# Performance work log

Measured on AMD Instinct MI355X. Metric: run time of the kernel, lower is better.

Reference implementation:

```python
import jax, jax.numpy as jnp
import numpy as np

B, S, D = 2, 2048, 2048
H, HD = 16, 128


def _rope_cos_sin(seq_len, head_dim, base=10000.0):
    inv_freq = 1.0 / (base ** (np.arange(0, head_dim, 2, dtype=np.float32) / head_dim))
    t = np.arange(seq_len, dtype=np.float32)
    freqs = np.outer(t, inv_freq)                      # [S, HD/2]
    emb = np.concatenate([freqs, freqs], axis=-1)      # [S, HD]
    return jnp.asarray(np.cos(emb)), jnp.asarray(np.sin(emb))


def setup_inputs() -> dict:
    key = jax.random.key(0)
    k1, k2, k3 = jax.random.split(key, 3)
    hidden_states = jax.random.normal(k1, (B, S, D), dtype=jnp.float32)
    cos, sin = _rope_cos_sin(S, HD)
    # qkv weight: [3, H*HD, D] as in CastedLinear(batch_output_dims=(3,))
    w_qkv = jax.random.normal(k2, (3, H * HD, D), dtype=jnp.float32) * (1.0 / D ** 0.5)
    w_o = jax.random.normal(k3, (D, H * HD), dtype=jnp.float32) * (1.0 / (H * HD) ** 0.5)
    return {"hidden_states": hidden_states, "cos": cos, "sin": sin, "w_qkv": w_qkv, "w_o": w_o}


def _rotate_half(x):
    x1, x2 = jnp.split(x, 2, axis=-1)
    return jnp.concatenate([-x2, x1], axis=-1)


def _apply_rope(x, cos, sin):
    # x: [B, S, H, HD]; cos/sin: [S, HD] -> broadcast over heads via [:, None, :]
    return x * cos[:, None, :] + _rotate_half(x) * sin[:, None, :]


def reference(hidden_states, cos, sin, w_qkv, w_o):
    # fused QKV projection: weight flattened to [3*H*HD, D]
    qkv = jnp.einsum('bsd,fd->bsf', hidden_states, w_qkv.reshape(-1, D))  # [B,S,3*H*HD]
    # rearrange '... (h hd) -> ... h hd' with h=H  ->  [B,S,H,3*HD], then chunk
    qkv = qkv.reshape(B, S, H, 3 * HD)
    q, k, v = jnp.split(qkv, 3, axis=-1)          # each [B,S,H,HD]
    q = _apply_rope(q, cos, sin)
    k = _apply_rope(k, cos, sin)
    # SDPA, causal
    scale = 1.0 / jnp.sqrt(jnp.asarray(HD, dtype=q.dtype))
    scores = jnp.einsum('bshd,bthd->bhst', q, k) * scale      # [B,H,S,S]
    causal = jnp.tril(jnp.ones((S, S), dtype=bool))
    scores = jnp.where(causal, scores, jnp.asarray(-jnp.inf, dtype=scores.dtype))
    probs = jax.nn.softmax(scores, axis=-1)
    attn = jnp.einsum('bhst,bthd->bshd', probs, v)            # [B,S,H,HD]
    attn = attn.reshape(B, S, H * HD)
    return jnp.einsum('bsf,df->bsd', attn, w_o)               # [B,S,D]
```

## Files before the change

kernel.cpp:

```cpp
#include <hip/hip_runtime.h>

typedef unsigned short u16;
typedef unsigned int u32;
typedef __bf16 bf16x8 __attribute__((ext_vector_type(8)));
typedef float f32x4 __attribute__((ext_vector_type(4)));


__device__ __forceinline__ u16 f2bf(float x) {
  __bf16 h = (__bf16)x;
  return __builtin_bit_cast(u16, h);
}

__device__ __forceinline__ void async_copy16(void* lds, const void* g) {
  __builtin_amdgcn_global_load_lds((const __attribute__((address_space(1))) void*)g,
                                   (__attribute__((address_space(3))) void*)lds, 16, 0, 0);
}

__global__ __launch_bounds__(256) void cast_all(const float* __restrict__ hidden,
                                                const float* __restrict__ wqkv,
                                                const float* __restrict__ wo,
                                                u16* __restrict__ xb,
                                                u16* __restrict__ wqb,
                                                u16* __restrict__ wob) {
  int i = blockIdx.x * 256 + threadIdx.x;
  const float* s;
  u16* d;
  int off;
  if (i < 2097152) { s = hidden; d = xb; off = i; }
  else if (i < 2097152 + 3145728) { s = wqkv; d = wqb; off = i - 2097152; }
  else { s = wo; d = wob; off = i - (2097152 + 3145728); }
  float4 v = ((const float4*)s)[off];
  ushort4 o;
  o.x = f2bf(v.x); o.y = f2bf(v.y); o.z = f2bf(v.z); o.w = f2bf(v.w);
  ((ushort4*)d)[off] = o;
}


__device__ __forceinline__ void lda_ks(bf16x8 (&af)[4][2], const u16* base, int row, int c,
                                       int ks) {
#pragma unroll
  for (int mf = 0; mf < 4; mf++) af[mf][ks] = *(const bf16x8*)(base + (row + mf * 16) * 64 + c);
}

__device__ __forceinline__ void ldb_ks(bf16x8 (&bfr)[2][2], const u16* base, int row, int c,
                                       int ks) {
#pragma unroll
  for (int nf = 0; nf < 2; nf++) bfr[nf][ks] = *(const bf16x8*)(base + (row + nf * 16) * 64 + c);
}

#define FENCE() asm volatile("" ::: "memory")
#define LGKM0() asm volatile("s_waitcnt lgkmcnt(0)" ::: "memory")
#define LGKM2() asm volatile("s_waitcnt lgkmcnt(2)" ::: "memory")
#define LGKM4() asm volatile("s_waitcnt lgkmcnt(4)" ::: "memory")
#define LGKM6() asm volatile("s_waitcnt lgkmcnt(6)" ::: "memory")
#define VMW6() asm volatile("s_waitcnt vmcnt(6)" ::: "memory")
#define VMW0() asm volatile("s_waitcnt vmcnt(0)" ::: "memory")
#define BAR() __builtin_amdgcn_s_barrier()
#define SBAR() __builtin_amdgcn_sched_barrier(0)

#define MFMA_H(MH, NH, KS)                                                               \
  _Pragma("unroll") for (int mf = 0; mf < 4; mf++)                                       \
  _Pragma("unroll") for (int nf = 0; nf < 2; nf++)                                       \
      acc[(MH)*4 + mf][(NH)*2 + nf] = __builtin_amdgcn_mfma_f32_16x16x32_bf16(           \
          af[mf][KS], bfr[nf][KS], acc[(MH)*4 + mf][(NH)*2 + nf], 0, 0, 0);

#define PH_SPLIT(MH, NH, W1, TAIL)      \
  BAR();                                \
  W1; SBAR();                           \
  __builtin_amdgcn_s_setprio(1);        \
  MFMA_H(MH, NH, 0);                    \
  LGKM0(); SBAR();                      \
  MFMA_H(MH, NH, 1);                    \
  __builtin_amdgcn_s_setprio(0);        \
  TAIL;                                 \
  FENCE(); BAR()

#define STG_A(DB, H, KT)                                                                   \
  {                                                                                        \
    async_copy16(ldsA + (DB)*32768 + ((H)*64 + w8) * 128, Ag + aoff[H][0] + (KT)*128);     \
    async_copy16(ldsA + (DB)*32768 + (128 + (H)*64 + w8) * 128, Ag + aoff[H][1] + (KT)*128); \
  }
#define STG_B(DB, H, KT)                                                                   \
  {                                                                                        \
    async_copy16(ldsB + (DB)*32768 + ((H)*64 + w8) * 128, Bg + boff[H][0] + (KT)*128);     \
    async_copy16(ldsB + (DB)*32768 + (128 + (H)*64 + w8) * 128, Bg + boff[H][1] + (KT)*128); \
  }

template <bool MORE>
__device__ __forceinline__ void qkv_iter(const u16* As, const u16* Bs, char* ldsA, char* ldsB,
                                         const char* Ag, const char* Bg,
                                         const u32 (&aoff)[2][2], const u32 (&boff)[2][2],
                                         int w8, int arow0, int brow0, int c0, int c1,
                                         int k1, int k2, int k3,
                                         bf16x8 (&af)[4][2], bf16x8 (&bfr)[2][2],
                                         f32x4 (&acc)[8][4]) {
  const int arow1 = arow0 + 256;
  const int brow1 = brow0 + 256;
  lda_ks(af, As, arow0, c0, 0); ldb_ks(bfr, Bs, brow0, c0, 0); FENCE();
  lda_ks(af, As, arow0, c1, 1); ldb_ks(bfr, Bs, brow0, c1, 1); FENCE();
  STG_B(1, 0, k1);
  PH_SPLIT(0, 0, LGKM6(), (void)0);
  ldb_ks(bfr, Bs, brow0 + 64, c0, 0); FENCE();
  ldb_ks(bfr, Bs, brow0 + 64, c1, 1); FENCE();
  if (MORE) { STG_A(0, 0, k2); }
  PH_SPLIT(0, 1, LGKM2(), (void)0);
  lda_ks(af, As, arow0 + 64, c0, 0); FENCE();
  lda_ks(af, As, arow0 + 64, c1, 1); FENCE();
  if (MORE) { STG_B(0, 1, k2); }
  PH_SPLIT(1, 1, LGKM4(), (void)0);
  ldb_ks(bfr, Bs, brow0, c0, 0); FENCE();
  ldb_ks(bfr, Bs, brow0, c1, 1); FENCE();
  if (MORE) { STG_A(0, 1, k2); }
  if (MORE) { PH_SPLIT(1, 0, LGKM2(), VMW6()); } else { PH_SPLIT(1, 0, LGKM2(), VMW0()); }
  lda_ks(af, As, arow1, c0, 0); ldb_ks(bfr, Bs, brow1, c0, 0); FENCE();
  lda_ks(af, As, arow1, c1, 1); ldb_ks(bfr, Bs, brow1, c1, 1); FENCE();
  if (MORE) { STG_B(0, 0, k2); }
  PH_SPLIT(0, 0, LGKM6(), (void)0);
  ldb_ks(bfr, Bs, brow1 + 64, c0, 0); FENCE();
  ldb_ks(bfr, Bs, brow1 + 64, c1, 1); FENCE();
  if (MORE) { STG_A(1, 0, k3); }
  PH_SPLIT(0, 1, LGKM2(), (void)0);
  lda_ks(af, As, arow1 + 64, c0, 0); FENCE();
  lda_ks(af, As, arow1 + 64, c1, 1); FENCE();
  if (MORE) { STG_B(1, 1, k3); }
  PH_SPLIT(1, 1, LGKM4(), (void)0);
  ldb_ks(bfr, Bs, brow1, c0, 0); FENCE();
  ldb_ks(bfr, Bs, brow1, c1, 1); FENCE();
  if (MORE) { STG_A(1, 1, k3); }
  if (MORE) { PH_SPLIT(1, 0, LGKM2(), VMW6()); } else { PH_SPLIT(1, 0, LGKM2(), (void)0); }
}

__global__ __launch_bounds__(512, 2) void gemm_qkv(const u16* __restrict__ A,
                                                   const u16* __restrict__ W,
                                                   const float* __restrict__ cosb,
                                                   const float* __restrict__ sinb,
                                                   u16* __restrict__ Qb,
                                                   u16* __restrict__ Kb,
                                                   u16* __restrict__ Vt) {
  extern __shared__ u16 smem[];
  u16* As = smem;
  u16* Bs = smem + 32768;
  char* ldsA = (char*)As;
  char* ldsB = (char*)Bs;
  const char* Ag = (const char*)A;
  const char* Bg = (const char*)W;

  const int tid = threadIdx.x;
  const int lane = tid & 63;
  const int w = tid >> 6;
  const int wm = w >> 2;
  const int wn = w & 3;
  const int r16 = lane & 15;
  const int g4 = lane >> 4;
  const int rsw = r16 & 7;
  const int w8 = w * 8;
  const int l8 = lane >> 3;
  const int gch = (lane & 7) ^ l8;

  const int nblk = blockIdx.x;
  const int swz = (nblk & 7) * 48 + (nblk >> 3);
  const int bm = (swz & 15) * 256;
  const int by = swz >> 4;
  const int bn = by * 256;

  u32 aoff[2][2], boff[2][2];
#pragma unroll
  for (int h = 0; h < 2; h++) {
#pragma unroll
    for (int j = 0; j < 2; j++) {
      int row = j * 128 + h * 64 + w8 + l8;
      aoff[h][j] = (u32)(bm + row) * 4096u + (u32)gch * 16u;
      boff[h][j] = (u32)(bn + row) * 4096u + (u32)gch * 16u;
    }
  }

  const int c0 = (g4 ^ rsw) * 8;
  const int c1 = ((4 + g4) ^ rsw) * 8;
  const int arow0 = wm * 128 + r16;
  const int brow0 = (wn >> 1) * 128 + (wn & 1) * 32 + r16;

  bf16x8 af[4][2], bfr[2][2];
  f32x4 acc[8][4];
  const f32x4 fzero = {0.0f, 0.0f, 0.0f, 0.0f};
#pragma unroll
  for (int i = 0; i < 8; i++)
#pragma unroll
    for (int j = 0; j < 4; j++) acc[i][j] = fzero;

  STG_A(0, 0, 0); STG_B(0, 0, 0); STG_B(0, 1, 0); STG_A(0, 1, 0);
  STG_A(1, 0, 1); STG_B(1, 1, 1); STG_A(1, 1, 1);
  VMW6();
  FENCE(); BAR();

#pragma unroll 1
  for (int t = 0; t < 15; t++) {
    qkv_iter<true>(As, Bs, ldsA, ldsB, Ag, Bg, aoff, boff, w8, arow0, brow0, c0, c1,
                   2 * t + 1, 2 * t + 2, 2 * t + 3, af, bfr, acc);
  }
  qkv_iter<false>(As, Bs, ldsA, ldsB, Ag, Bg, aoff, boff, w8, arow0, brow0, c0, c1,
                  31, 31, 31, af, bfr, acc);

  const int blk128 = by * 2 + (wn >> 1);
  const int which = blk128 % 3;
  const int head = blk128 / 3;
  const float qs = (which == 0) ? 0.08838834764831845f * 1.4426950408889634f : 1.0f;
  const int hb = (wn & 1) * 32;

#pragma unroll
  for (int mi = 0; mi < 8; mi++) {
#pragma unroll
    for (int r = 0; r < 4; r++) {
      int row = bm + wm * 128 + mi * 16 + g4 * 4 + r;
      int bb = row >> 11;
      int s = row & 2047;
      size_t bhIdx = (size_t)(bb * 16 + head);
      if (which == 2) {
#pragma unroll
        for (int ni = 0; ni < 4; ni++) {
          int hd = hb + (ni & 1) * 16 + (ni >> 1) * 64 + r16;
          Vt[(bhIdx * 128 + hd) * 2048 + s] = f2bf(acc[mi][ni][r]);
        }
      } else {
        u16* dst = (which ? Kb : Qb) + (bhIdx * 2048 + (size_t)s) * 128;
#pragma unroll
        for (int ni = 0; ni < 2; ni++) {
          int hd = hb + ni * 16 + r16;
          float c = cosb[s * 128 + hd] * qs;
          float sn = sinb[s * 128 + hd] * qs;
          float x1 = acc[mi][ni][r], x2 = acc[mi][ni + 2][r];
          dst[hd] = f2bf(x1 * c - x2 * sn);
          dst[hd + 64] = f2bf(x2 * c + x1 * sn);
        }
      }
    }
  }
}

#undef STG_A
#undef STG_B
#undef MFMA_H
#undef PH_SPLIT

__global__ __launch_bounds__(512) void flash_attn(const u16* __restrict__ Q,
                                                  const u16* __restrict__ K,
                                                  const u16* __restrict__ Vt,
                                                  u16* __restrict__ O) {
  __shared__ __align__(16) u16 Ks[2][128 * 128];
  __shared__ __align__(16) u16 Vs[2][128 * 128];
  __shared__ __align__(16) u16 Ps[8 * 16 * 64];
  const int tid = threadIdx.x;
  const int lane = tid & 63;
  const int wave = tid >> 6;
  const int bh = blockIdx.y;
  const int r16 = lane & 15;
  const int g4 = lane >> 4;
  const int rsw = r16 & 7;
  const u16* Qh = Q + (size_t)bh * 2048 * 128;
  const u16* Kh = K + (size_t)bh * 2048 * 128;
  const u16* Vh = Vt + (size_t)bh * 128 * 2048;
  const int b = bh >> 4;
  const int h = bh & 15;

  int koff[4], voff[4], ldsOff[4];
#pragma unroll
  for (int i = 0; i < 4; i++) {
    int r = (wave * 4 + i) * 4 + (lane >> 4);
    int c = (lane & 15) ^ (r & 7);
    koff[i] = r * 128 + c * 8;
    voff[i] = r * 2048 + c * 8;
    ldsOff[i] = (wave * 4 + i) * 512;
  }

#pragma unroll 1
  for (int pass = 0; pass < 2; pass++) {
    const int T = pass == 0 ? (int)blockIdx.x : 15 - (int)blockIdx.x;
    const int qg = T * 128 + wave * 16 + r16;
    const int nk = T + 1;

    bf16x8 qf[4];
#pragma unroll
    for (int ks = 0; ks < 4; ks++)
      qf[ks] = *(const bf16x8*)(Qh + (size_t)qg * 128 + ks * 32 + g4 * 8);

    f32x4 o[8];
    f32x4 zero = {0.0f, 0.0f, 0.0f, 0.0f};
#pragma unroll
    for (int c = 0; c < 8; c++) o[c] = zero;
    float m_i = -__builtin_inff();
    float l_i = 0.0f;

    __syncthreads();
#pragma unroll
    for (int i = 0; i < 4; i++) {
      async_copy16(&Ks[0][ldsOff[i]], Kh + koff[i]);
      async_copy16(&Vs[0][ldsOff[i]], Vh + voff[i]);
    }

    int cur = 0;
    for (int u = 0; u < nk; u++) {
      __syncthreads();
      if (u + 1 < nk) {
#pragma unroll
        for (int i = 0; i < 4; i++) {
          async_copy16(&Ks[cur ^ 1][ldsOff[i]], Kh + (size_t)(u + 1) * 16384 + koff[i]);
          async_copy16(&Vs[cur ^ 1][ldsOff[i]], Vh + (size_t)(u + 1) * 128 + voff[i]);
        }
      }

      f32x4 sacc[8];
#pragma unroll
      for (int n = 0; n < 8; n++) sacc[n] = zero;
#pragma unroll
      for (int n = 0; n < 8; n++) {
#pragma unroll
        for (int ks = 0; ks < 4; ks++) {
          bf16x8 kf = *(const bf16x8*)(&Ks[cur][(n * 16 + r16) * 128 + ((ks * 4 + g4) ^ rsw) * 8]);
          sacc[n] = __builtin_amdgcn_mfma_f32_16x16x32_bf16(kf, qf[ks], sacc[n], 0, 0, 0);
        }
      }

      if (u == nk - 1) {
#pragma unroll
        for (int n = 0; n < 8; n++)
#pragma unroll
          for (int r = 0; r < 4; r++) {
            int key = u * 128 + 16 * n + g4 * 4 + r;
            if (key > qg) sacc[n][r] = -__builtin_inff();
          }
      }
      float vmax = -__builtin_inff();
#pragma unroll
      for (int n = 0; n < 8; n++)
#pragma unroll
        for (int r = 0; r < 4; r++) vmax = fmaxf(vmax, sacc[n][r]);
      vmax = fmaxf(vmax, __shfl_xor(vmax, 16));
      vmax = fmaxf(vmax, __shfl_xor(vmax, 32));
      float mn = fmaxf(m_i, vmax);
      float alpha = exp2f(m_i - mn);
      m_i = mn;

#pragma unroll
      for (int c = 0; c < 8; c++)
#pragma unroll
        for (int r = 0; r < 4; r++) o[c][r] *= alpha;

      float ssum = 0.0f;
      u16* Pw = &Ps[wave * 1024];
#pragma unroll
      for (int half = 0; half < 2; half++) {
#pragma unroll
        for (int nl = 0; nl < 4; nl++) {
          int n = half * 4 + nl;
          float p0 = exp2f(sacc[n][0] - mn);
          float p1 = exp2f(sacc[n][1] - mn);
          float p2 = exp2f(sacc[n][2] - mn);
          float p3 = exp2f(sacc[n][3] - mn);
          ssum += (p0 + p1) + (p2 + p3);
          ushort4 pk;
          pk.x = f2bf(p0); pk.y = f2bf(p1); pk.z = f2bf(p2); pk.w = f2bf(p3);
          *(ushort4*)(&Pw[r16 * 64 + ((2 * nl + (g4 >> 1)) ^ rsw) * 8 + (g4 & 1) * 4]) = pk;
        }
#pragma unroll
        for (int ks2 = 0; ks2 < 2; ks2++) {
          bf16x8 pf = *(const bf16x8*)(&Pw[r16 * 64 + ((ks2 * 4 + g4) ^ rsw) * 8]);
          int kv = half * 2 + ks2;
#pragma unroll
          for (int c = 0; c < 8; c++) {
            bf16x8 vf = *(const bf16x8*)(&Vs[cur][(c * 16 + r16) * 128 + ((kv * 4 + g4) ^ rsw) * 8]);
            o[c] = __builtin_amdgcn_mfma_f32_16x16x32_bf16(vf, pf, o[c], 0, 0, 0);
          }
        }
      }
      ssum += __shfl_xor(ssum, 16);
      ssum += __shfl_xor(ssum, 32);
      l_i = l_i * alpha + ssum;
      cur ^= 1;
    }

    float rl = 1.0f / l_i;
    u16* dst = O + ((size_t)(b * 2048 + qg)) * 2048 + h * 128;
#pragma unroll
    for (int c = 0; c < 8; c++) {
      ushort4 pk;
      pk.x = f2bf(o[c][0] * rl);
      pk.y = f2bf(o[c][1] * rl);
      pk.z = f2bf(o[c][2] * rl);
      pk.w = f2bf(o[c][3] * rl);
      *(ushort4*)(dst + c * 16 + g4 * 4) = pk;
    }
  }
}

__global__ __launch_bounds__(256) void gemm_out(const u16* __restrict__ A,
                                                const u16* __restrict__ W,
                                                float* __restrict__ out) {
  __shared__ __align__(16) u16 As[128 * 64];
  __shared__ __align__(16) u16 Bs[128 * 64];
  const int tid = threadIdx.x;
  const int lane = tid & 63;
  const int wave = tid >> 6;
  const int wm = (wave >> 1) * 64;
  const int wn = (wave & 1) * 64;
  const int r16 = lane & 15;
  const int g4 = lane >> 4;
  const int rsw = r16 & 7;
  const int bm = blockIdx.x * 128;
  const int bn = blockIdx.y * 128;

  size_t aoff[4], boff[4];
  u16* ldsA[4];
  u16* ldsB[4];
#pragma unroll
  for (int i = 0; i < 4; i++) {
    int row = wave * 32 + i * 8 + (lane >> 3);
    int c = (lane & 7) ^ (row & 7);
    aoff[i] = (size_t)(bm + row) * 2048 + c * 8;
    boff[i] = (size_t)(bn + row) * 2048 + c * 8;
    ldsA[i] = &As[(wave * 4 + i) * 512];
    ldsB[i] = &Bs[(wave * 4 + i) * 512];
  }

  f32x4 acc[4][4];
  f32x4 zero = {0.0f, 0.0f, 0.0f, 0.0f};
#pragma unroll
  for (int m = 0; m < 4; m++)
#pragma unroll
    for (int n = 0; n < 4; n++) acc[m][n] = zero;

  for (int kt = 0; kt < 2048; kt += 64) {
    __syncthreads();
#pragma unroll
    for (int i = 0; i < 4; i++) {
      async_copy16(ldsA[i], A + aoff[i] + kt);
      async_copy16(ldsB[i], W + boff[i] + kt);
    }
    __syncthreads();
#pragma unroll
    for (int ks = 0; ks < 2; ks++) {
      bf16x8 af[4], bfr[4];
#pragma unroll
      for (int m = 0; m < 4; m++)
        af[m] = *(const bf16x8*)(&As[(wm + m * 16 + r16) * 64 + ((ks * 4 + g4) ^ rsw) * 8]);
#pragma unroll
      for (int n = 0; n < 4; n++)
        bfr[n] = *(const bf16x8*)(&Bs[(wn + n * 16 + r16) * 64 + ((ks * 4 + g4) ^ rsw) * 8]);
#pragma unroll
      for (int m = 0; m < 4; m++)
#pragma unroll
        for (int n = 0; n < 4; n++)
          acc[m][n] = __builtin_amdgcn_mfma_f32_16x16x32_bf16(af[m], bfr[n], acc[m][n], 0, 0, 0);
    }
  }

#pragma unroll
  for (int m = 0; m < 4; m++) {
#pragma unroll
    for (int n = 0; n < 4; n++) {
#pragma unroll
      for (int r = 0; r < 4; r++) {
        int row = bm + wm + m * 16 + g4 * 4 + r;
        int col = bn + wn + n * 16 + r16;
        out[(size_t)row * 2048 + col] = acc[m][n][r];
      }
    }
  }
}

extern "C" void kernel_launch(void* const* d_in, const int* in_sizes, int n_in,
                              void* d_out, int out_size, void* d_ws, size_t ws_size,
                              hipStream_t stream) {
  const float* hidden = (const float*)d_in[0];
  const float* cosb   = (const float*)d_in[1];
  const float* sinb   = (const float*)d_in[2];
  const float* w_qkv  = (const float*)d_in[3];
  const float* w_o    = (const float*)d_in[4];
  float* out = (float*)d_out;

  char* ws = (char*)d_ws;
  u16* Xbf    = (u16*)(ws);
  u16* Wqkvbf = (u16*)(ws + 16777216);
  u16* Wobf   = (u16*)(ws + 41943040);
  u16* Qb     = (u16*)(ws + 50331648);
  u16* Kb     = (u16*)(ws + 67108864);
  u16* Vt     = (u16*)(ws + 83886080);
  u16* Ob     = (u16*)(ws + 100663296);

  static int attr_done = 0;
  if (!attr_done) {
    (void)hipFuncSetAttribute((const void*)gemm_qkv,
                              hipFuncAttributeMaxDynamicSharedMemorySize, 131072);
    attr_done = 1;
  }

  cast_all<<<24576, 256, 0, stream>>>(hidden, w_qkv, w_o, Xbf, Wqkvbf, Wobf);
  gemm_qkv<<<384, 512, 131072, stream>>>(Xbf, Wqkvbf, cosb, sinb, Qb, Kb, Vt);
  flash_attn<<<dim3(8, 32), 512, 0, stream>>>(Qb, Kb, Vt, Ob);
  gemm_out<<<dim3(32, 16), 256, 0, stream>>>(Ob, Wobf, out);
}
```

Measured before the change: 387.3 us.

## Rebalance QKV GEMM to 256 blocks with split half-tile tail work

The QKV GEMM grid shrinks from 384 to 256 workgroups, matching the CU count. Each block first computes one full 256x256 tile covering output columns 0-4095. It then computes a 128x256 half-tile from the remaining column range (tiles 16-23), split along M across two blocks. The aim is to remove the wave-quantization tail of 384 tiles over 256 CUs, at the cost of a simpler, less pipelined double-buffered loop for the half-tile phase.

```diff
diff --git a/kernel.cpp b/kernel.cpp
--- a/kernel.cpp
+++ b/kernel.cpp
@@ -64,6 +64,13 @@
       acc[(MH)*4 + mf][(NH)*2 + nf] = __builtin_amdgcn_mfma_f32_16x16x32_bf16(           \
           af[mf][KS], bfr[nf][KS], acc[(MH)*4 + mf][(NH)*2 + nf], 0, 0, 0);
 
+#define MFMA_HALF(NB)                                                                    \
+  _Pragma("unroll") for (int ks = 0; ks < 2; ks++)                                       \
+  _Pragma("unroll") for (int mf = 0; mf < 4; mf++)                                       \
+  _Pragma("unroll") for (int nf = 0; nf < 2; nf++)                                       \
+      acc[mf][(NB) + nf] = __builtin_amdgcn_mfma_f32_16x16x32_bf16(                      \
+          af[mf][ks], bfr[nf][ks], acc[mf][(NB) + nf], 0, 0, 0);
+
 #define PH_SPLIT(MH, NH, W1, TAIL)      \
   BAR();                                \
   W1; SBAR();                           \
@@ -84,6 +91,16 @@
   {                                                                                        \
     async_copy16(ldsB + (DB)*32768 + ((H)*64 + w8) * 128, Bg + boff[H][0] + (KT)*128);     \
     async_copy16(ldsB + (DB)*32768 + (128 + (H)*64 + w8) * 128, Bg + boff[H][1] + (KT)*128); \
+  }
+#define STG_AH(DB, KT)                                                                     \
+  {                                                                                        \
+    async_copy16(ldsA + (DB)*32768 + (w8) * 128, Ag + aoffH[0] + (KT)*128);                \
+    async_copy16(ldsA + (DB)*32768 + (64 + w8) * 128, Ag + aoffH[1] + (KT)*128);           \
+  }
+#define STG_BH(DB, H, KT)                                                                  \
+  {                                                                                        \
+    async_copy16(ldsB + (DB)*32768 + ((H)*64 + w8) * 128, Bg + boffH[H][0] + (KT)*128);    \
+    async_copy16(ldsB + (DB)*32768 + (128 + (H)*64 + w8) * 128, Bg + boffH[H][1] + (KT)*128); \
   }
 
 template <bool MORE>
@@ -158,7 +175,8 @@
   const int gch = (lane & 7) ^ l8;
 
   const int nblk = blockIdx.x;
-  const int swz = (nblk & 7) * 48 + (nblk >> 3);
+  const int swz = (nblk & 7) * 32 + (nblk >> 3);
+
   const int bm = (swz & 15) * 256;
   const int by = swz >> 4;
   const int bn = by * 256;
@@ -200,45 +218,141 @@
   qkv_iter<false>(As, Bs, ldsA, ldsB, Ag, Bg, aoff, boff, w8, arow0, brow0, c0, c1,
                   31, 31, 31, af, bfr, acc);
 
-  const int blk128 = by * 2 + (wn >> 1);
-  const int which = blk128 % 3;
-  const int head = blk128 / 3;
-  const float qs = (which == 0) ? 0.08838834764831845f * 1.4426950408889634f : 1.0f;
-  const int hb = (wn & 1) * 32;
-
-#pragma unroll
-  for (int mi = 0; mi < 8; mi++) {
-#pragma unroll
-    for (int r = 0; r < 4; r++) {
-      int row = bm + wm * 128 + mi * 16 + g4 * 4 + r;
-      int bb = row >> 11;
-      int s = row & 2047;
-      size_t bhIdx = (size_t)(bb * 16 + head);
-      if (which == 2) {
-#pragma unroll
-        for (int ni = 0; ni < 4; ni++) {
-          int hd = hb + (ni & 1) * 16 + (ni >> 1) * 64 + r16;
-          Vt[(bhIdx * 128 + hd) * 2048 + s] = f2bf(acc[mi][ni][r]);
-        }
-      } else {
-        u16* dst = (which ? Kb : Qb) + (bhIdx * 2048 + (size_t)s) * 128;
-#pragma unroll
-        for (int ni = 0; ni < 2; ni++) {
-          int hd = hb + ni * 16 + r16;
-          float c = cosb[s * 128 + hd] * qs;
-          float sn = sinb[s * 128 + hd] * qs;
-          float x1 = acc[mi][ni][r], x2 = acc[mi][ni + 2][r];
-          dst[hd] = f2bf(x1 * c - x2 * sn);
-          dst[hd + 64] = f2bf(x2 * c + x1 * sn);
+  {
+    const int blk128 = by * 2 + (wn >> 1);
+    const int which = blk128 % 3;
+    const int head = blk128 / 3;
+    const float qs = (which == 0) ? 0.08838834764831845f * 1.4426950408889634f : 1.0f;
+    const int hb = (wn & 1) * 32;
+
+#pragma unroll
+    for (int mi = 0; mi < 8; mi++) {
+#pragma unroll
+      for (int r = 0; r < 4; r++) {
+        int row = bm + wm * 128 + mi * 16 + g4 * 4 + r;
+        int bb = row >> 11;
+        int s = row & 2047;
+        size_t bhIdx = (size_t)(bb * 16 + head);
+        if (which == 2) {
+#pragma unroll
+          for (int ni = 0; ni < 4; ni++) {
+            int hd = hb + (ni & 1) * 16 + (ni >> 1) * 64 + r16;
+            Vt[(bhIdx * 128 + hd) * 2048 + s] = f2bf(acc[mi][ni][r]);
+          }
+        } else {
+          u16* dst = (which ? Kb : Qb) + (bhIdx * 2048 + (size_t)s) * 128;
+#pragma unroll
+          for (int ni = 0; ni < 2; ni++) {
+            int hd = hb + ni * 16 + r16;
+            float c = cosb[s * 128 + hd] * qs;
+            float sn = sinb[s * 128 + hd] * qs;
+            float x1 = acc[mi][ni][r], x2 = acc[mi][ni + 2][r];
+            dst[hd] = f2bf(x1 * c - x2 * sn);
+            dst[hd + 64] = f2bf(x2 * c + x1 * sn);
+          }
         }
       }
     }
   }
+
+  const int hbm = swz & 15;
+  const int hby = 16 + ((swz >> 4) & 7);
+  const int mh = swz >> 7;
+  const int hbn = hby * 256;
+
+  u32 aoffH[2];
+#pragma unroll
+  for (int j = 0; j < 2; j++)
+    aoffH[j] = (u32)(hbm * 256 + mh * 128 + j * 64 + w8 + l8) * 4096u + (u32)gch * 16u;
+  u32 boffH[2][2];
+#pragma unroll
+  for (int h = 0; h < 2; h++)
+#pragma unroll
+    for (int j = 0; j < 2; j++)
+      boffH[h][j] = (u32)(hbn + j * 128 + h * 64 + w8 + l8) * 4096u + (u32)gch * 16u;
+
+#pragma unroll
+  for (int i = 0; i < 4; i++)
+#pragma unroll
+    for (int j = 0; j < 4; j++) acc[i][j] = fzero;
+
+  const int arowH = wm * 64 + r16;
+
+  STG_AH(0, 0); STG_BH(0, 0, 0); STG_BH(0, 1, 0);
+
+#pragma unroll 1
+  for (int kt = 0; kt < 32; kt++) {
+    const int db = kt & 1;
+    const u16* AsH = smem + db * 16384;
+    const u16* BsH = smem + 32768 + db * 16384;
+    FENCE(); BAR();
+    if (kt < 31) {
+      STG_AH(db ^ 1, kt + 1); STG_BH(db ^ 1, 0, kt + 1); STG_BH(db ^ 1, 1, kt + 1);
+      VMW6();
+    } else {
+      VMW0();
+    }
+    FENCE(); BAR();
+    lda_ks(af, AsH, arowH, c0, 0);
+    lda_ks(af, AsH, arowH, c1, 1);
+    ldb_ks(bfr, BsH, brow0, c0, 0);
+    ldb_ks(bfr, BsH, brow0, c1, 1);
+    LGKM0(); SBAR();
+    __builtin_amdgcn_s_setprio(1);
+    MFMA_HALF(0);
+    __builtin_amdgcn_s_setprio(0);
+    ldb_ks(bfr, BsH, brow0 + 64, c0, 0);
+    ldb_ks(bfr, BsH, brow0 + 64, c1, 1);
+    LGKM0(); SBAR();
+    __builtin_amdgcn_s_setprio(1);
+    MFMA_HALF(2);
+    __builtin_amdgcn_s_setprio(0);
+  }
+
+  {
+    const int blk128 = hby * 2 + (wn >> 1);
+    const int which = blk128 % 3;
+    const int head = blk128 / 3;
+    const float qs = (which == 0) ? 0.08838834764831845f * 1.4426950408889634f : 1.0f;
+    const int hb = (wn & 1) * 32;
+
+#pragma unroll
+    for (int mi = 0; mi < 4; mi++) {
+#pragma unroll
+      for (int r = 0; r < 4; r++) {
+        int row = hbm * 256 + mh * 128 + wm * 64 + mi * 16 + g4 * 4 + r;
+        int bb = row >> 11;
+        int s = row & 2047;
+        size_t bhIdx = (size_t)(bb * 16 + head);
+        if (which == 2) {
+#pragma unroll
+          for (int ni = 0; ni < 4; ni++) {
+            int hd = hb + (ni & 1) * 16 + (ni >> 1) * 64 + r16;
+            Vt[(bhIdx * 128 + hd) * 2048 + s] = f2bf(acc[mi][ni][r]);
+          }
+        } else {
+          u16* dst = (which ? Kb : Qb) + (bhIdx * 2048 + (size_t)s) * 128;
+#pragma unroll
+          for (int ni = 0; ni < 2; ni++) {
+            int hd = hb + ni * 16 + r16;
+            float c = cosb[s * 128 + hd] * qs;
+            float sn = sinb[s * 128 + hd] * qs;
+            float x1 = acc[mi][ni][r], x2 = acc[mi][ni + 2][r];
+            dst[hd] = f2bf(x1 * c - x2 * sn);
+            dst[hd + 64] = f2bf(x2 * c + x1 * sn);
+          }
+        }
+      }
+    }
+  }
 }
 
 #undef STG_A
 #undef STG_B
+#undef STG_AH
+#undef STG_BH
 #undef MFMA_H
+#undef MFMA_HALF
 #undef PH_SPLIT
 
 __global__ __launch_bounds__(512) void flash_attn(const u16* __restrict__ Q,
@@ -493,7 +607,7 @@
   }
 
   cast_all<<<24576, 256, 0, stream>>>(hidden, w_qkv, w_o, Xbf, Wqkvbf, Wobf);
-  gemm_qkv<<<384, 512, 131072, stream>>>(Xbf, Wqkvbf, cosb, sinb, Qb, Kb, Vt);
+  gemm_qkv<<<256, 512, 131072, stream>>>(Xbf, Wqkvbf, cosb, sinb, Qb, Kb, Vt);
   flash_attn<<<dim3(8, 32), 512, 0, stream>>>(Qb, Kb, Vt, Ob);
   gemm_out<<<dim3(32, 16), 256, 0, stream>>>(Ob, Wobf, out);
 }
```

Result: faster. 369.0 us (-4.7%).
